# Optimization experiments

Hardware: AMD Instinct MI355X
Metric: run time of the kernel (lower is better)

The kernel has to match this reference:

```python
import jax, jax.numpy as jnp
import numpy as np

N, E = 4096, 131072
IN_DIM, HID, H = 128, 64, 8
D = HID * H          # 512 = d_model
DFF = HID * 4        # 256 (source uses hidden_dim*4, not d_model*4)
NEG_SLOPE = 0.2
LN_EPS = 1e-5


def setup_inputs() -> dict:
    key = jax.random.key(0)
    ks = jax.random.split(key, 24)
    r = lambda i, shp, s=0.05: (jax.random.normal(ks[i], shp, jnp.float32) * s)
    return {
        "x": jax.random.normal(ks[0], (N, IN_DIM), jnp.float32),
        "edge_index": jax.random.randint(ks[1], (2, E), 0, N, dtype=jnp.int32),
        "batch": jnp.zeros((N,), jnp.int32),
        "gat_lin_w": r(2, (D, IN_DIM)),
        "gat_att_src": r(3, (H, HID)),
        "gat_att_dst": r(4, (H, HID)),
        "gat_bias": jnp.zeros((D,), jnp.float32),
        "qkv_w": r(5, (2, 3 * D, D)),
        "qkv_b": jnp.zeros((2, 3 * D), jnp.float32),
        "out_w": r(6, (2, D, D)),
        "out_b": jnp.zeros((2, D), jnp.float32),
        "ln1_g": jnp.ones((2, D), jnp.float32),
        "ln1_b": jnp.zeros((2, D), jnp.float32),
        "ff1_w": r(7, (2, DFF, D)),
        "ff1_b": jnp.zeros((2, DFF), jnp.float32),
        "ff2_w": r(8, (2, D, DFF)),
        "ff2_b": jnp.zeros((2, D), jnp.float32),
        "ln2_g": jnp.ones((2, D), jnp.float32),
        "ln2_b": jnp.zeros((2, D), jnp.float32),
    }


def _layer_norm(x, g, b):
    mu = jnp.mean(x, -1, keepdims=True)
    var = jnp.mean(jnp.square(x - mu), -1, keepdims=True)
    return (x - mu) * jax.lax.rsqrt(var + LN_EPS) * g + b


def _gat(x, edge_index, lin_w, att_src, att_dst, bias):
    # PyG GATConv: linear -> per-edge leaky_relu attention -> softmax over dst -> scatter-add
    h = (x @ lin_w.T).reshape(N, H, HID)                 # [N,H,C]
    loops = jnp.arange(N, dtype=edge_index.dtype)        # add_self_loops=True (PyG default)
    src = jnp.concatenate([edge_index[0], loops])
    dst = jnp.concatenate([edge_index[1], loops])
    a_src = jnp.einsum('nhc,hc->nh', h, att_src)         # [N,H]
    a_dst = jnp.einsum('nhc,hc->nh', h, att_dst)
    e = jax.nn.leaky_relu(a_src[src] + a_dst[dst], NEG_SLOPE)   # [E+N,H]
    emax = jax.ops.segment_max(e, dst, num_segments=N)          # self-loops => no empty segment
    p = jnp.exp(e - emax[dst])
    denom = jax.ops.segment_sum(p, dst, num_segments=N)
    alpha = p / (denom[dst] + 1e-16)                             # [E+N,H]
    msg = alpha[..., None] * h[src]                              # [E+N,H,C]
    out = jax.ops.segment_sum(msg, dst, num_segments=N)         # [N,H,C]
    return out.reshape(N, D) + bias


def _mha(x, w_qkv, b_qkv, w_o, b_o):
    qkv = x @ w_qkv.T + b_qkv                            # [N,3D]
    q, k, v = jnp.split(qkv, 3, axis=-1)
    q = q.reshape(N, H, HID).transpose(1, 0, 2)          # [H,N,c]
    k = k.reshape(N, H, HID).transpose(1, 0, 2)
    v = v.reshape(N, H, HID).transpose(1, 0, 2)
    scores = jnp.einsum('hnc,hmc->hnm', q, k) / jnp.sqrt(jnp.float32(HID))
    attn = jax.nn.softmax(scores, axis=-1)
    o = jnp.einsum('hnm,hmc->hnc', attn, v).transpose(1, 0, 2).reshape(N, D)
    return o @ w_o.T + b_o


def reference(x, edge_index, batch, gat_lin_w, gat_att_src, gat_att_dst, gat_bias,
              qkv_w, qkv_b, out_w, out_b, ln1_g, ln1_b,
              ff1_w, ff1_b, ff2_w, ff2_b, ln2_g, ln2_b):
    h = _gat(x, edge_index, gat_lin_w, gat_att_src, gat_att_dst, gat_bias)
    # TransformerEncoder, 2 post-norm layers, relu FFN, dropout=0; seq_len=N, batch=1
    for i in range(2):
        a = _mha(h, qkv_w[i], qkv_b[i], out_w[i], out_b[i])
        h = _layer_norm(h + a, ln1_g[i], ln1_b[i])
        f = jax.nn.relu(h @ ff1_w[i].T + ff1_b[i]) @ ff2_w[i].T + ff2_b[i]
        h = _layer_norm(h + f, ln2_g[i], ln2_b[i])
    return h
```

## Files before the change

kernel.cpp:

```cpp
#include <hip/hip_runtime.h>
#include <math.h>

#define NN    4096
#define EE    131072
#define ENE   (EE + NN)
#define IND   128
#define HH    8
#define HIDC  64
#define DD    512
#define D3    1536
#define DFF2  256

typedef __attribute__((ext_vector_type(8))) short short8;
typedef __attribute__((ext_vector_type(4))) float f32x4;
typedef __attribute__((ext_vector_type(2))) unsigned int uint2v;

__device__ __forceinline__ float lrelu02(float x) { return x >= 0.f ? x : 0.2f * x; }

__device__ __forceinline__ unsigned short f2bf(float x) {
    unsigned int u = __float_as_uint(x);
    u += 0x7fffu + ((u >> 16) & 1u);
    return (unsigned short)(u >> 16);
}
__device__ __forceinline__ float bf2f(unsigned short u) {
    return __uint_as_float((unsigned int)u << 16);
}
__device__ __forceinline__ unsigned int cvt_pk_bf16(float lo, float hi) {
    unsigned int r;
    asm("v_cvt_pk_bf16_f32 %0, %1, %2" : "=v"(r) : "v"(lo), "v"(hi));
    return r;
}
__device__ __forceinline__ float max3f(float a, float b, float c) {
    float r;
    asm("v_max3_f32 %0, %1, %2, %3" : "=v"(r) : "v"(a), "v"(b), "v"(c));
    return r;
}

struct CvtJobs {
    const float* src[6];
    unsigned short* dst[6];
    int n[6];
};

__global__ __launch_bounds__(256) void cvt_many(CvtJobs jb, int total)
{
    int i = (blockIdx.x * 256 + threadIdx.x) * 4;
    if (i >= total) return;
    int s = 0;
    while (i >= jb.n[s]) { i -= jb.n[s]; ++s; }
    float4 v = *(const float4*)(jb.src[s] + i);
    unsigned int lo = (unsigned int)f2bf(v.x) | ((unsigned int)f2bf(v.y) << 16);
    unsigned int hi = (unsigned int)f2bf(v.z) | ((unsigned int)f2bf(v.w) << 16);
    uint2v pk; pk.x = lo; pk.y = hi;
    *(uint2v*)(jb.dst[s] + i) = pk;
}

__global__ __launch_bounds__(256) void gemm64(const unsigned short* __restrict__ A,
                                              const unsigned short* __restrict__ W,
                                              const float* __restrict__ bias,
                                              void* __restrict__ C,
                                              int M, int K, int N, int flags)
{
    __shared__ __align__(16) unsigned short As[64 * 64];
    __shared__ __align__(16) unsigned short Bs[64 * 64];

    const int t = threadIdx.x, lane = t & 63, w = t >> 6;
    const int wr = w >> 1, wc = w & 1;
    const int bm = blockIdx.y * 64, bn = blockIdx.x * 64;
    const int q = lane & 15, g = lane >> 4;

    f32x4 acc[2][2];
#pragma unroll
    for (int m = 0; m < 2; ++m)
#pragma unroll
        for (int n = 0; n < 2; ++n) acc[m][n] = (f32x4){0.f, 0.f, 0.f, 0.f};

    const int srow = t >> 2, sh = t & 3;
    const unsigned short* Ag = A + (size_t)(bm + srow) * K + sh * 16;
    const unsigned short* Wg = W + (size_t)(bn + srow) * K + sh * 16;
    int wofs[2];
#pragma unroll
    for (int i = 0; i < 2; ++i)
        wofs[i] = srow * 128 + ((((sh * 2 + i) * 16) ^ ((srow & 7) << 4)));

    for (int k0 = 0; k0 < K; k0 += 64) {
        short8 av[2], bv[2];
#pragma unroll
        for (int i = 0; i < 2; ++i) {
            av[i] = *(const short8*)(Ag + k0 + i * 8);
            bv[i] = *(const short8*)(Wg + k0 + i * 8);
        }
        __syncthreads();
#pragma unroll
        for (int i = 0; i < 2; ++i) {
            *(short8*)((char*)As + wofs[i]) = av[i];
            *(short8*)((char*)Bs + wofs[i]) = bv[i];
        }
        __syncthreads();

        short8 af[2][2], bfr[2][2];
#pragma unroll
        for (int m = 0; m < 2; ++m) {
            const int row = wr * 32 + m * 16 + q;
#pragma unroll
            for (int kk = 0; kk < 2; ++kk)
                af[kk][m] = *(const short8*)((const char*)As +
                    row * 128 + ((((kk * 4 + g) * 16) ^ ((row & 7) << 4))));
        }
#pragma unroll
        for (int n = 0; n < 2; ++n) {
            const int row = wc * 32 + n * 16 + q;
#pragma unroll
            for (int kk = 0; kk < 2; ++kk)
                bfr[kk][n] = *(const short8*)((const char*)Bs +
                    row * 128 + ((((kk * 4 + g) * 16) ^ ((row & 7) << 4))));
        }
#pragma unroll
        for (int kk = 0; kk < 2; ++kk)
#pragma unroll
            for (int m = 0; m < 2; ++m)
#pragma unroll
                for (int n = 0; n < 2; ++n)
                    acc[m][n] = __builtin_amdgcn_mfma_f32_16x16x32_bf16(
                        bfr[kk][n], af[kk][m], acc[m][n], 0, 0, 0);
    }

    const int obf = flags & 1, orelu = flags & 2, oqs = flags & 4;
#pragma unroll
    for (int m = 0; m < 2; ++m) {
        const int row = bm + wr * 32 + m * 16 + q;
#pragma unroll
        for (int n = 0; n < 2; ++n) {
            const int col0 = bn + wc * 32 + n * 16 + g * 4;
            f32x4 v = acc[m][n];
            if (bias) {
                float4 bv4 = *(const float4*)(bias + col0);
                v[0] += bv4.x; v[1] += bv4.y; v[2] += bv4.z; v[3] += bv4.w;
            }
            if (oqs && col0 < DD) {
                const float qs = 0.18033688f;
                v[0] *= qs; v[1] *= qs; v[2] *= qs; v[3] *= qs;
            }
            if (orelu) {
                v[0] = fmaxf(v[0], 0.f); v[1] = fmaxf(v[1], 0.f);
                v[2] = fmaxf(v[2], 0.f); v[3] = fmaxf(v[3], 0.f);
            }
            if (obf) {
                uint2v pk;
                pk.x = (unsigned int)f2bf(v[0]) | ((unsigned int)f2bf(v[1]) << 16);
                pk.y = (unsigned int)f2bf(v[2]) | ((unsigned int)f2bf(v[3]) << 16);
                *(uint2v*)((unsigned short*)C + (size_t)row * N + col0) = pk;
            } else {
                float4 o; o.x = v[0]; o.y = v[1]; o.z = v[2]; o.w = v[3];
                *(float4*)((float*)C + (size_t)row * N + col0) = o;
            }
        }
    }
}

__global__ void att_proj(const unsigned short* __restrict__ hlin,
                         const float* __restrict__ att_s,
                         const float* __restrict__ att_d,
                         float* __restrict__ a_src, float* __restrict__ a_dst)
{
    int idx = blockIdx.x * 256 + threadIdx.x;
    if (idx >= NN * HH) return;
    int n = idx >> 3, h = idx & 7;
    const unsigned short* hp = hlin + (size_t)n * DD + h * HIDC;
    const float* as = att_s + h * HIDC;
    const float* ad = att_d + h * HIDC;
    float s1 = 0.f, s2 = 0.f;
#pragma unroll 8
    for (int c = 0; c < HIDC; ++c) {
        float hv = bf2f(hp[c]);
        s1 += hv * as[c]; s2 += hv * ad[c];
    }
    a_src[idx] = s1;
    a_dst[idx] = s2;
}

__global__ void hist_kernel(const int* __restrict__ ei, int* __restrict__ counts)
{
    int i = blockIdx.x * 256 + threadIdx.x;
    if (i >= ENE) return;
    int dst = (i < EE) ? ei[EE + i] : (i - EE);
    atomicAdd(&counts[dst], 1);
}

__global__ __launch_bounds__(1024) void scan_kernel(const int* __restrict__ counts,
                                                    int* __restrict__ offsets)
{
    __shared__ int sums[1024];
    int t = threadIdx.x;
    int v0 = counts[t*4+0], v1 = counts[t*4+1], v2 = counts[t*4+2], v3 = counts[t*4+3];
    sums[t] = v0 + v1 + v2 + v3;
    __syncthreads();
    for (int off = 1; off < 1024; off <<= 1) {
        int x = (t >= off) ? sums[t - off] : 0;
        __syncthreads();
        sums[t] += x;
        __syncthreads();
    }
    int pre = (t > 0) ? sums[t-1] : 0;
    offsets[t*4+0] = pre;
    offsets[t*4+1] = pre + v0;
    offsets[t*4+2] = pre + v0 + v1;
    offsets[t*4+3] = pre + v0 + v1 + v2;
    if (t == 1023) offsets[4096] = sums[1023];
}

__global__ void scatter_kernel(const int* __restrict__ ei, const int* __restrict__ offs,
                               int* __restrict__ cursor, int* __restrict__ src_sorted)
{
    int i = blockIdx.x * 256 + threadIdx.x;
    if (i >= ENE) return;
    int s, d;
    if (i < EE) { s = ei[i]; d = ei[EE + i]; } else { s = d = i - EE; }
    int pos = atomicAdd(&cursor[d], 1);
    src_sorted[offs[d] + pos] = s;
}

__global__ __launch_bounds__(256) void gat_node(const unsigned short* __restrict__ hlin,
                                                const float* __restrict__ a_src,
                                                const float* __restrict__ a_dst,
                                                const int* __restrict__ offs,
                                                const int* __restrict__ src_sorted,
                                                const float* __restrict__ bias,
                                                float* __restrict__ out,
                                                unsigned short* __restrict__ outb)
{
    __shared__ float adst[8];
    __shared__ float emax[8];
    __shared__ float denom[8];
    __shared__ float red[256];
    __shared__ float p_lds[16][8];
    __shared__ int   srcs[16];

    const int n = blockIdx.x, t = threadIdx.x;
    if (t < 8) { adst[t] = a_dst[n * 8 + t]; denom[t] = 0.f; }
    const int off0 = offs[n];
    const int deg  = offs[n+1] - off0;
    __syncthreads();

    const int h = t & 7, slot = t >> 3;
    float mx = -3.0e38f;
    for (int j = slot; j < deg; j += 32) {
        int s = src_sorted[off0 + j];
        mx = fmaxf(mx, a_src[s * 8 + h] + adst[h]);
    }
    red[t] = mx;
    __syncthreads();
    for (int half = 128; half >= 8; half >>= 1) {
        if (t < half) red[t] = fmaxf(red[t], red[t + half]);
        __syncthreads();
    }
    if (t < 8) emax[t] = lrelu02(red[t]);
    __syncthreads();

    float acc0 = 0.f, acc1 = 0.f;
    const int h0 = t >> 6, h1 = (t + 256) >> 6;
    for (int base = 0; base < deg; base += 16) {
        int cnt = min(16, deg - base);
        if (t < cnt * 8) {
            int j = base + (t >> 3);
            int s = src_sorted[off0 + j];
            if ((t & 7) == 0) srcs[t >> 3] = s;
            float x = a_src[s * 8 + (t & 7)] + adst[t & 7];
            float p = __expf(lrelu02(x) - emax[t & 7]);
            p_lds[t >> 3][t & 7] = p;
            atomicAdd(&denom[t & 7], p);
        }
        __syncthreads();
        for (int jj = 0; jj < cnt; ++jj) {
            int s = srcs[jj];
            const unsigned short* hp = hlin + (size_t)s * DD;
            acc0 += p_lds[jj][h0] * bf2f(hp[t]);
            acc1 += p_lds[jj][h1] * bf2f(hp[256 + t]);
        }
        __syncthreads();
    }
    float o0 = acc0 / (denom[h0] + 1e-16f) + bias[t];
    float o1 = acc1 / (denom[h1] + 1e-16f) + bias[256 + t];
    out[(size_t)n * DD + t]        = o0;
    out[(size_t)n * DD + 256 + t]  = o1;
    outb[(size_t)n * DD + t]       = f2bf(o0);
    outb[(size_t)n * DD + 256 + t] = f2bf(o1);
}

#define KVB 128
#define NTT (NN / KVB)

__global__ __launch_bounds__(256) void attn_mfma(const unsigned short* __restrict__ qkv,
                                                 unsigned short* __restrict__ aob)
{
    __shared__ __align__(16) unsigned short Ks0[KVB * 64];
    __shared__ __align__(16) unsigned short Vt0[80 * KVB];
    __shared__ __align__(16) unsigned short Ks1[KVB * 64];
    __shared__ __align__(16) unsigned short Vt1[80 * KVB];

    const int t = threadIdx.x;
    const int w = t >> 6, lane = t & 63;
    const int q15 = lane & 15, g = lane >> 4;

    const int fid = blockIdx.x;
    const int h = fid & 7, qb = fid >> 3;
    const int qbase = qb * 64 + w * 16;

    const unsigned short* qrow = qkv + (size_t)(qbase + q15) * D3 + h * HIDC;
    const short8 qf0 = *(const short8*)(qrow + g * 8);
    const short8 qf1 = *(const short8*)(qrow + 32 + g * 8);

    f32x4 O[4];
#pragma unroll
    for (int db = 0; db < 4; ++db) O[db] = (f32x4){0.f, 0.f, 0.f, 0.f};
    f32x4 O5 = (f32x4){0.f, 0.f, 0.f, 0.f};
    float m_run = -3.0e38f;

    int koff[8][2];
#pragma unroll
    for (int kvb = 0; kvb < 8; ++kvb) {
        const int kr = kvb * 16 + q15;
        koff[kvb][0] = (kr * 64 + g * 8) ^ ((kr & 7) << 3);
        koff[kvb][1] = (kr * 64 + 32 + g * 8) ^ ((kr & 7) << 3);
    }
    int voff[4][4];
#pragma unroll
    for (int db = 0; db < 4; ++db) {
        const int vr = db * 16 + q15;
#pragma unroll
        for (int ks = 0; ks < 4; ++ks)
            voff[db][ks] = (vr * KVB + ks * 32 + g * 8) ^ ((vr & 7) << 3);
    }
    int voffE[4];
#pragma unroll
    for (int ks = 0; ks < 4; ++ks) {
        const int rv = 64 + q15;
        voffE[ks] = (rv * KVB + ks * 32 + g * 8) ^ ((rv & 7) << 3);
    }
    const int kr_s = t >> 1, sh = t & 1;
    const int kq = t & 31, dg = t >> 5;
    const int slot4 = (kq >> 3) * 32 + (kq & 3) * 8 + ((kq >> 2) & 1) * 4;
    int kwoff[4];
#pragma unroll
    for (int i = 0; i < 4; ++i)
        kwoff[i] = (kr_s * 64 + (sh * 4 + i) * 8) ^ ((kr_s & 7) << 3);
    int vwoff[8];
#pragma unroll
    for (int i = 0; i < 8; ++i) {
        const int d = dg * 8 + i;
        vwoff[i] = (d * KVB + slot4) ^ ((d & 7) << 3);
    }
    const unsigned short* Kg = qkv + (size_t)kr_s * D3 + DD + h * HIDC + sh * 32;
    const unsigned short* Vg = qkv + (size_t)(4 * kq) * D3 + 2 * DD + h * HIDC + dg * 8;

    short8 kreg[4], vreg[4];

    auto LOAD_KV = [&](int kb) {
        const size_t off = (size_t)kb * KVB * D3;
#pragma unroll
        for (int i = 0; i < 4; ++i) kreg[i] = *(const short8*)(Kg + off + i * 8);
#pragma unroll
        for (int jj = 0; jj < 4; ++jj) vreg[jj] = *(const short8*)(Vg + off + (size_t)jj * D3);
    };
    auto WRITE_KV = [&](unsigned short* KD, unsigned short* VD) {
#pragma unroll
        for (int i = 0; i < 4; ++i)
            *(short8*)&KD[kwoff[i]] = kreg[i];
        const unsigned int* w0 = (const unsigned int*)&vreg[0];
        const unsigned int* w1 = (const unsigned int*)&vreg[1];
        const unsigned int* w2 = (const unsigned int*)&vreg[2];
        const unsigned int* w3 = (const unsigned int*)&vreg[3];
#pragma unroll
        for (int i = 0; i < 8; ++i) {
            const unsigned int sel = (i & 1) ? 0x07060302u : 0x05040100u;
            uint2v pk;
            pk.x = __builtin_amdgcn_perm(w1[i >> 1], w0[i >> 1], sel);
            pk.y = __builtin_amdgcn_perm(w3[i >> 1], w2[i >> 1], sel);
            *(uint2v*)&VD[vwoff[i]] = pk;
        }
    };

    auto TILE = [&](int kb, const unsigned short* BK, const unsigned short* BV,
                    unsigned short* NK, unsigned short* NV) {
        const int kbn = kb + 1;
        if (kbn < NTT) LOAD_KV(kbn);

        f32x4 st[8];
        __builtin_amdgcn_s_setprio(1);
#pragma unroll
        for (int kvb = 0; kvb < 8; ++kvb) {
            const short8 kf0 = *(const short8*)&BK[koff[kvb][0]];
            const short8 kf1 = *(const short8*)&BK[koff[kvb][1]];
            f32x4 acc = (f32x4){0.f, 0.f, 0.f, 0.f};
            acc = __builtin_amdgcn_mfma_f32_16x16x32_bf16(kf0, qf0, acc, 0, 0, 0);
            acc = __builtin_amdgcn_mfma_f32_16x16x32_bf16(kf1, qf1, acc, 0, 0, 0);
            st[kvb] = acc;
        }
        __builtin_amdgcn_s_setprio(0);

        float pm0 = max3f(st[0][0], st[0][1], st[0][2]);
        float pm1 = max3f(st[0][3], st[1][0], st[1][1]);
        float pm2 = max3f(st[1][2], st[1][3], st[2][0]);
        float pm3 = max3f(st[2][1], st[2][2], st[2][3]);
        float pm4 = max3f(st[3][0], st[3][1], st[3][2]);
        float pm5 = max3f(st[3][3], st[4][0], st[4][1]);
        float pm6 = max3f(st[4][2], st[4][3], st[5][0]);
        float pm7 = max3f(st[5][1], st[5][2], st[5][3]);
        float pm8 = max3f(st[6][0], st[6][1], st[6][2]);
        float pm9 = max3f(st[6][3], st[7][0], st[7][1]);
        float pmA = max3f(st[7][2], st[7][3], pm0);
        float q0 = max3f(pm1, pm2, pm3);
        float q1 = max3f(pm4, pm5, pm6);
        float q2 = max3f(pm7, pm8, pm9);
        float pmax = max3f(q0, q1, q2);
        pmax = fmaxf(pmax, pmA);
        pmax = fmaxf(pmax, __shfl_xor(pmax, 16, 64));
        pmax = fmaxf(pmax, __shfl_xor(pmax, 32, 64));
        if (!__all(pmax <= m_run + 11.f)) {
            const float mnew = fmaxf(m_run, pmax);
            const float f = exp2f(m_run - mnew);
#pragma unroll
            for (int db = 0; db < 4; ++db) O[db] *= f;
            O5 *= f;
            m_run = mnew;
        }

        short8 pf[4];
#pragma unroll
        for (int ks = 0; ks < 4; ++ks) {
            float e0 = exp2f(st[2*ks  ][0] - m_run), e1 = exp2f(st[2*ks  ][1] - m_run);
            float e2 = exp2f(st[2*ks  ][2] - m_run), e3 = exp2f(st[2*ks  ][3] - m_run);
            float e4 = exp2f(st[2*ks+1][0] - m_run), e5 = exp2f(st[2*ks+1][1] - m_run);
            float e6 = exp2f(st[2*ks+1][2] - m_run), e7 = exp2f(st[2*ks+1][3] - m_run);
            union { unsigned int u[4]; short8 s8; } pu;
            pu.u[0] = cvt_pk_bf16(e0, e1);
            pu.u[1] = cvt_pk_bf16(e2, e3);
            pu.u[2] = cvt_pk_bf16(e4, e5);
            pu.u[3] = cvt_pk_bf16(e6, e7);
            pf[ks] = pu.s8;
        }

        __builtin_amdgcn_s_setprio(1);
#pragma unroll
        for (int db = 0; db < 4; ++db) {
#pragma unroll
            for (int ks = 0; ks < 4; ++ks) {
                const short8 vf = *(const short8*)&BV[voff[db][ks]];
                O[db] = __builtin_amdgcn_mfma_f32_16x16x32_bf16(vf, pf[ks], O[db], 0, 0, 0);
            }
        }
#pragma unroll
        for (int ks = 0; ks < 4; ++ks) {
            const short8 vfE = *(const short8*)&BV[voffE[ks]];
            O5 = __builtin_amdgcn_mfma_f32_16x16x32_bf16(vfE, pf[ks], O5, 0, 0, 0);
        }
        __builtin_amdgcn_s_setprio(0);

        if (kbn < NTT) {
            WRITE_KV(NK, NV);
            __syncthreads();
        }
    };

    {
        const int d = 64 + (t >> 4), c = (t & 15) * 8;
        short8 iv;
#pragma unroll
        for (int i = 0; i < 8; ++i)
            iv[i] = (short)((d == 64) ? 0x3F80 : 0);
        const int ofs = (d * KVB + c) ^ ((d & 7) << 3);
        *(short8*)&Vt0[ofs] = iv;
        *(short8*)&Vt1[ofs] = iv;
    }
    LOAD_KV(0);
    WRITE_KV(Ks0, Vt0);
    __syncthreads();

    for (int kb = 0; kb < NTT; kb += 2) {
        TILE(kb,     Ks0, Vt0, Ks1, Vt1);
        TILE(kb + 1, Ks1, Vt1, Ks0, Vt0);
    }

    const float lsum = __shfl(O5[0], q15, 64);
    const float linv = 1.f / lsum;
#pragma unroll
    for (int db = 0; db < 4; ++db) {
        uint2v pk;
        pk.x = (unsigned int)f2bf(O[db][0] * linv) | ((unsigned int)f2bf(O[db][1] * linv) << 16);
        pk.y = (unsigned int)f2bf(O[db][2] * linv) | ((unsigned int)f2bf(O[db][3] * linv) << 16);
        *(uint2v*)&aob[(size_t)(qbase + q15) * DD + h * HIDC + db * 16 + g * 4] = pk;
    }
}

__global__ __launch_bounds__(256) void ln_fused(const float* __restrict__ hin,
                                                const unsigned short* __restrict__ dlt,
                                                const float* __restrict__ g,
                                                const float* __restrict__ b,
                                                float* __restrict__ out,
                                                unsigned short* __restrict__ outb)
{
    __shared__ float red[256];
    const int r = blockIdx.x, t = threadIdx.x;
    const size_t base = (size_t)r * DD;
    float2 hv = *(const float2*)(hin + base + 2 * t);
    unsigned int dv = *(const unsigned int*)(dlt + base + 2 * t);
    float v0 = hv.x + bf2f((unsigned short)(dv & 0xffffu));
    float v1 = hv.y + bf2f((unsigned short)(dv >> 16));
    red[t] = v0 + v1;
    __syncthreads();
    for (int off = 128; off > 0; off >>= 1) { if (t < off) red[t] += red[t + off]; __syncthreads(); }
    float mu = red[0] * (1.f / 512.f);
    __syncthreads();
    float d0 = v0 - mu, d1 = v1 - mu;
    red[t] = d0 * d0 + d1 * d1;
    __syncthreads();
    for (int off = 128; off > 0; off >>= 1) { if (t < off) red[t] += red[t + off]; __syncthreads(); }
    float rs = rsqrtf(red[0] * (1.f / 512.f) + 1e-5f);
    float2 gv = *(const float2*)(g + 2 * t);
    float2 bv = *(const float2*)(b + 2 * t);
    float o0 = d0 * rs * gv.x + bv.x;
    float o1 = d1 * rs * gv.y + bv.y;
    float2 ov; ov.x = o0; ov.y = o1;
    *(float2*)(out + base + 2 * t) = ov;
    if (outb) {
        unsigned int pk = (unsigned int)f2bf(o0) | ((unsigned int)f2bf(o1) << 16);
        *(unsigned int*)(outb + base + 2 * t) = pk;
    }
}

extern "C" void kernel_launch(void* const* d_in, const int* in_sizes, int n_in,
                              void* d_out, int out_size, void* d_ws, size_t ws_size,
                              hipStream_t stream)
{
    (void)in_sizes; (void)n_in; (void)out_size; (void)ws_size;

    const float* x        = (const float*)d_in[0];
    const int*   ei       = (const int*)  d_in[1];
    const float* lin_w    = (const float*)d_in[3];
    const float* att_src  = (const float*)d_in[4];
    const float* att_dst  = (const float*)d_in[5];
    const float* gat_bias = (const float*)d_in[6];
    const float* qkv_w    = (const float*)d_in[7];
    const float* qkv_b    = (const float*)d_in[8];
    const float* out_w    = (const float*)d_in[9];
    const float* out_b    = (const float*)d_in[10];
    const float* ln1_g    = (const float*)d_in[11];
    const float* ln1_b    = (const float*)d_in[12];
    const float* ff1_w    = (const float*)d_in[13];
    const float* ff1_b    = (const float*)d_in[14];
    const float* ff2_w    = (const float*)d_in[15];
    const float* ff2_b    = (const float*)d_in[16];
    const float* ln2_g    = (const float*)d_in[17];
    const float* ln2_b    = (const float*)d_in[18];

    char* wsb = (char*)d_ws;
    size_t o = 0;
    auto alloc = [&](size_t bytes) { char* p = wsb + o; o += (bytes + 255) & ~(size_t)255; return p; };

    unsigned short* hlin_bf = (unsigned short*)alloc((size_t)NN * DD * 2);
    unsigned short* hbf     = (unsigned short*)alloc((size_t)NN * DD * 2);
    unsigned short* qkv16   = (unsigned short*)alloc((size_t)NN * D3 * 2);
    unsigned short* aob     = (unsigned short*)alloc((size_t)NN * DD * 2);
    unsigned short* ff1obf  = (unsigned short*)alloc((size_t)NN * DFF2 * 2);
    unsigned short* dltbf   = (unsigned short*)alloc((size_t)NN * DD * 2);
    float* hcur  = (float*)alloc((size_t)NN * DD * 4);
    float* a_src = (float*)alloc((size_t)NN * HH * 4);
    float* a_dst = (float*)alloc((size_t)NN * HH * 4);
    int* counts     = (int*)alloc(NN * 4);
    int* cursor     = (int*)alloc(NN * 4);
    int* offsets    = (int*)alloc((NN + 1) * 4);
    int* src_sorted = (int*)alloc(ENE * 4);
    unsigned short* xbf    = (unsigned short*)alloc((size_t)NN * IND * 2);
    unsigned short* linwbf = (unsigned short*)alloc((size_t)DD * IND * 2);
    unsigned short* qkvwbf = (unsigned short*)alloc((size_t)2 * D3 * DD * 2);
    unsigned short* outwbf = (unsigned short*)alloc((size_t)2 * DD * DD * 2);
    unsigned short* ff1wbf = (unsigned short*)alloc((size_t)2 * DFF2 * DD * 2);
    unsigned short* ff2wbf = (unsigned short*)alloc((size_t)2 * DD * DFF2 * 2);

    CvtJobs jb;
    jb.src[0] = x;      jb.dst[0] = xbf;    jb.n[0] = NN * IND;
    jb.src[1] = lin_w;  jb.dst[1] = linwbf; jb.n[1] = DD * IND;
    jb.src[2] = qkv_w;  jb.dst[2] = qkvwbf; jb.n[2] = 2 * D3 * DD;
    jb.src[3] = out_w;  jb.dst[3] = outwbf; jb.n[3] = 2 * DD * DD;
    jb.src[4] = ff1_w;  jb.dst[4] = ff1wbf; jb.n[4] = 2 * DFF2 * DD;
    jb.src[5] = ff2_w;  jb.dst[5] = ff2wbf; jb.n[5] = 2 * DD * DFF2;
    int cvt_total = jb.n[0]+jb.n[1]+jb.n[2]+jb.n[3]+jb.n[4]+jb.n[5];
    cvt_many<<<(cvt_total/4 + 255)/256, 256, 0, stream>>>(jb, cvt_total);

    hipMemsetAsync(counts, 0, 2 * NN * sizeof(int), stream);
    gemm64<<<dim3(DD/64, NN/64), 256, 0, stream>>>(xbf, linwbf, nullptr, hlin_bf,
                                                   NN, IND, DD, 1);
    att_proj<<<(NN*HH + 255)/256, 256, 0, stream>>>(hlin_bf, att_src, att_dst, a_src, a_dst);
    hist_kernel<<<(ENE + 255)/256, 256, 0, stream>>>(ei, counts);
    scan_kernel<<<1, 1024, 0, stream>>>(counts, offsets);
    scatter_kernel<<<(ENE + 255)/256, 256, 0, stream>>>(ei, offsets, cursor, src_sorted);
    gat_node<<<NN, 256, 0, stream>>>(hlin_bf, a_src, a_dst, offsets, src_sorted, gat_bias,
                                     hcur, hbf);

    for (int i = 0; i < 2; ++i) {
        gemm64<<<dim3(D3/64, NN/64), 256, 0, stream>>>(hbf, qkvwbf + (size_t)i*D3*DD,
                                                       qkv_b + (size_t)i*D3, qkv16,
                                                       NN, DD, D3, 1 | 4);
        attn_mfma<<<dim3(NN/64 * HH), 256, 0, stream>>>(qkv16, aob);
        gemm64<<<dim3(DD/64, NN/64), 256, 0, stream>>>(aob, outwbf + (size_t)i*DD*DD,
                                                       out_b + (size_t)i*DD, dltbf,
                                                       NN, DD, DD, 1);
        ln_fused<<<NN, 256, 0, stream>>>(hcur, dltbf, ln1_g + (size_t)i*DD, ln1_b + (size_t)i*DD,
                                         hcur, hbf);
        gemm64<<<dim3(DFF2/64, NN/64), 256, 0, stream>>>(hbf, ff1wbf + (size_t)i*DFF2*DD,
                                                         ff1_b + (size_t)i*DFF2, ff1obf,
                                                         NN, DD, DFF2, 1 | 2);
        gemm64<<<dim3(DD/64, NN/64), 256, 0, stream>>>(ff1obf, ff2wbf + (size_t)i*DD*DFF2,
                                                       ff2_b + (size_t)i*DD, dltbf,
                                                       NN, DFF2, DD, 1);
        float* outp = (i == 1) ? (float*)d_out : hcur;
        unsigned short* outbp = (i == 1) ? nullptr : hbf;
        ln_fused<<<NN, 256, 0, stream>>>(hcur, dltbf, ln2_g + (size_t)i*DD, ln2_b + (size_t)i*DD,
                                         outp, outbp);
    }
}
```

Before: 329.9 us.

## Software-pipeline flash attention: compute next tile's QK before current softmax/PV

```diff
diff --git a/kernel.cpp b/kernel.cpp
--- a/kernel.cpp
+++ b/kernel.cpp
@@ -380,12 +380,7 @@
         }
     };
 
-    auto TILE = [&](int kb, const unsigned short* BK, const unsigned short* BV,
-                    unsigned short* NK, unsigned short* NV) {
-        const int kbn = kb + 1;
-        if (kbn < NTT) LOAD_KV(kbn);
-
-        f32x4 st[8];
+    auto QK = [&](const unsigned short* BK, f32x4* dst) {
         __builtin_amdgcn_s_setprio(1);
 #pragma unroll
         for (int kvb = 0; kvb < 8; ++kvb) {
@@ -394,10 +389,12 @@
             f32x4 acc = (f32x4){0.f, 0.f, 0.f, 0.f};
             acc = __builtin_amdgcn_mfma_f32_16x16x32_bf16(kf0, qf0, acc, 0, 0, 0);
             acc = __builtin_amdgcn_mfma_f32_16x16x32_bf16(kf1, qf1, acc, 0, 0, 0);
-            st[kvb] = acc;
+            dst[kvb] = acc;
         }
         __builtin_amdgcn_s_setprio(0);
-
+    };
+
+    auto SMPV = [&](f32x4* st, const unsigned short* BV) {
         float pm0 = max3f(st[0][0], st[0][1], st[0][2]);
         float pm1 = max3f(st[0][3], st[1][0], st[1][1]);
         float pm2 = max3f(st[1][2], st[1][3], st[2][0]);
@@ -409,10 +406,10 @@
         float pm8 = max3f(st[6][0], st[6][1], st[6][2]);
         float pm9 = max3f(st[6][3], st[7][0], st[7][1]);
         float pmA = max3f(st[7][2], st[7][3], pm0);
-        float q0 = max3f(pm1, pm2, pm3);
-        float q1 = max3f(pm4, pm5, pm6);
-        float q2 = max3f(pm7, pm8, pm9);
-        float pmax = max3f(q0, q1, q2);
+        float r0 = max3f(pm1, pm2, pm3);
+        float r1 = max3f(pm4, pm5, pm6);
+        float r2 = max3f(pm7, pm8, pm9);
+        float pmax = max3f(r0, r1, r2);
         pmax = fmaxf(pmax, pmA);
         pmax = fmaxf(pmax, __shfl_xor(pmax, 16, 64));
         pmax = fmaxf(pmax, __shfl_xor(pmax, 32, 64));
@@ -455,9 +452,19 @@
             O5 = __builtin_amdgcn_mfma_f32_16x16x32_bf16(vfE, pf[ks], O5, 0, 0, 0);
         }
         __builtin_amdgcn_s_setprio(0);
-
-        if (kbn < NTT) {
-            WRITE_KV(NK, NV);
+    };
+
+    auto STEP = [&](int kb, unsigned short* CK, unsigned short* CV,
+                    const unsigned short* NK, const unsigned short* NV,
+                    f32x4* stc, f32x4* stn) {
+        (void)NV;
+        const int kbn = kb + 1, kbw = kb + 2;
+        if (kbw < NTT) LOAD_KV(kbw);
+        if (kbn < NTT) QK(NK, stn);
+        SMPV(stc, CV);
+        if (kbw < NTT) {
+            __syncthreads();
+            WRITE_KV(CK, CV);
             __syncthreads();
         }
     };
@@ -472,13 +479,18 @@
         *(short8*)&Vt0[ofs] = iv;
         *(short8*)&Vt1[ofs] = iv;
     }
+    f32x4 st_a[8], st_b[8];
     LOAD_KV(0);
     WRITE_KV(Ks0, Vt0);
     __syncthreads();
+    LOAD_KV(1);
+    QK(Ks0, st_a);
+    WRITE_KV(Ks1, Vt1);
+    __syncthreads();
 
     for (int kb = 0; kb < NTT; kb += 2) {
-        TILE(kb,     Ks0, Vt0, Ks1, Vt1);
-        TILE(kb + 1, Ks1, Vt1, Ks0, Vt0);
+        STEP(kb,     Ks0, Vt0, Ks1, Vt1, st_a, st_b);
+        STEP(kb + 1, Ks1, Vt1, Ks0, Vt0, st_b, st_a);
     }
 
     const float lsum = __shfl(O5[0], q15, 64);
```

After: 434.5 us. +31.7%, slower.
